# Performance work log

Hardware: AMD Instinct MI355X
Metric: run time of the kernel (lower is better)

The kernel has to match this reference:

```python
import jax, jax.numpy as jnp
import numpy as np


def setup_inputs() -> dict:
    key = jax.random.key(0)
    k1, k2 = jax.random.split(key)
    feat1 = jax.random.normal(k1, (4, 256, 64, 64), dtype=jnp.float32)
    feat2 = jax.random.normal(k2, (4, 256, 64, 64), dtype=jnp.float32)
    return {"feat1": feat1, "feat2": feat2}


def reference(feat1, feat2):
    b, c, h, w = feat1.shape
    hw = h * w
    f1 = feat1.reshape(b, c, hw)  # (b, c, hw)
    f2 = feat2.reshape(b, c, hw)  # (b, c, hw)
    # all-pairs dot-product correlation: corr[b, i, j] = sum_c f1[b,c,i] * f2[b,c,j]
    corr = jnp.einsum('bci,bcj->bij', f1, f2)  # (b, hw, hw)
    # softmax over query-position axis i (torch dim=1)
    out = jax.nn.softmax(corr, axis=1)
    return out.reshape(b, hw, h, w)
```

## Files before the change

kernel.cpp:

```cpp
#include <hip/hip_runtime.h>
#include <math.h>
#include <stdint.h>

#define HW 4096
#define NC 256
#define NB 4
#define NT 32

#define BM 128
#define BN 128
#define BK 32
#define LDP 40

typedef _Float16 f16;
typedef _Float16 half8 __attribute__((ext_vector_type(8)));
typedef float f32x4 __attribute__((ext_vector_type(4)));

#define GLD16(gp, lp) __builtin_amdgcn_global_load_lds( \
    (const __attribute__((address_space(1))) void*)(gp), \
    (__attribute__((address_space(3))) void*)(lp), 16, 0, 0)

__global__ __launch_bounds__(256) void split_tile(const float* __restrict__ src,
                                                  f16* __restrict__ dh,
                                                  f16* __restrict__ dl) {
    const int it = blockIdx.x;
    const int kt = blockIdx.y;
    const int b  = blockIdx.z;
    const float* S = src + (size_t)b * NC * HW + (size_t)kt * 32 * HW + it * 128;

    __shared__ float st[32][133];
    const int t = threadIdx.x;

    {
        const int i4 = (t & 31) * 4;
        const int c0 = t >> 5;
#pragma unroll
        for (int p = 0; p < 4; ++p) {
            const int c = c0 + p * 8;
            const float4 v = *(const float4*)&S[(size_t)c * HW + i4];
            st[c][i4] = v.x; st[c][i4 + 1] = v.y;
            st[c][i4 + 2] = v.z; st[c][i4 + 3] = v.w;
        }
    }
    __syncthreads();

    const size_t tile_base = ((size_t)b * 256 + (size_t)it * 8 + kt) * (128 * 32);
#pragma unroll
    for (int p = 0; p < 2; ++p) {
        const int cid = t + p * 256;
        const int r = cid >> 2, ch = cid & 3;
        f16 h8[8], l8[8];
#pragma unroll
        for (int q = 0; q < 8; ++q) {
            const float x = st[ch * 8 + q][r];
            h8[q] = (f16)x;
            l8[q] = (f16)(x - (float)h8[q]);
        }
        const int off = r * 32 + ((ch ^ ((r >> 1) & 3)) << 3);
        *(half8*)&dh[tile_base + off] = *(half8*)&h8[0];
        *(half8*)&dl[tile_base + off] = *(half8*)&l8[0];
    }
}

__global__ __launch_bounds__(256) void gemm_corr_mfma_t(const f16* __restrict__ Ah,
                                                        const f16* __restrict__ Al,
                                                        const f16* __restrict__ Bh,
                                                        const f16* __restrict__ Bl,
                                                        float* __restrict__ corr,
                                                        f16* __restrict__ p16,
                                                        const int use16,
                                                        float* __restrict__ pm,
                                                        float* __restrict__ ps) {
    const int flat = blockIdx.y * 32 + blockIdx.x;
    const int swz  = (flat & 7) * 128 + (flat >> 3);
    const int it = swz & 31;
    const int jt = swz >> 5;
    const int b  = blockIdx.z;
    const int i0 = it * BM;
    const int j0 = jt * BN;
    float* Cp  = corr + (size_t)b * HW * HW;
    f16*   Pp  = p16  + (size_t)b * HW * HW;

    __shared__ __align__(16) f16 sAh[2 * 4096];
    __shared__ __align__(16) f16 sAl[2 * 4096];
    __shared__ __align__(16) f16 sBh[2 * 4096];
    __shared__ __align__(16) f16 sBl[2 * 4096];

    const int t    = threadIdx.x;
    const int lane = t & 63;
    const int wave = t >> 6;
    const int wr   = (wave >> 1) * 64;
    const int wc   = (wave & 1) * 64;
    const int fm   = lane & 15;
    const int ca   = lane >> 4;

    const size_t abase = ((size_t)b * 256 + (size_t)it * 8) * 4096;
    const size_t bbase = ((size_t)b * 256 + (size_t)jt * 8) * 4096;

    const int swzk = (fm >> 1) & 3;
    const int cswz = ((ca ^ swzk) << 3);
    int aoff[4], boff[4];
#pragma unroll
    for (int u = 0; u < 4; ++u) aoff[u] = (wr + u * 16 + fm) * 32 + cswz;
#pragma unroll
    for (int v = 0; v < 4; ++v) boff[v] = (wc + v * 16 + fm) * 32 + cswz;

    f32x4 acc[4][4];
#pragma unroll
    for (int u = 0; u < 4; ++u)
#pragma unroll
        for (int v = 0; v < 4; ++v) acc[u][v] = (f32x4)(0.f);

    const int stg = wave * 1024 + lane * 8;

#define STAGE(buf, kt_) do {                                             \
        const size_t koff_ = (size_t)(kt_) * 4096;                       \
        _Pragma("unroll")                                                \
        for (int p_ = 0; p_ < 2; ++p_) {                                 \
            const int h_  = stg + p_ * 512;                              \
            const int lb_ = (buf) * 4096 + (wave * 2 + p_) * 512;        \
            GLD16(Ah + abase + koff_ + h_, &sAh[lb_]);                   \
            GLD16(Al + abase + koff_ + h_, &sAl[lb_]);                   \
            GLD16(Bh + bbase + koff_ + h_, &sBh[lb_]);                   \
            GLD16(Bl + bbase + koff_ + h_, &sBl[lb_]);                   \
        }                                                                \
    } while (0)

    STAGE(0, 0);
    __syncthreads();

#pragma unroll
    for (int kt = 0; kt < NC / BK; ++kt) {
        const int cur = kt & 1;
        if (kt < NC / BK - 1) STAGE(cur ^ 1, kt + 1);

        const int cb = cur * 4096;
        half8 fah[4], fal[4], fbh[4], fbl[4];
#pragma unroll
        for (int u = 0; u < 4; ++u) {
            fah[u] = *(const half8*)&sAh[cb + aoff[u]];
            fal[u] = *(const half8*)&sAl[cb + aoff[u]];
        }
#pragma unroll
        for (int v = 0; v < 4; ++v) {
            fbh[v] = *(const half8*)&sBh[cb + boff[v]];
            fbl[v] = *(const half8*)&sBl[cb + boff[v]];
        }
#pragma unroll
        for (int u = 0; u < 4; ++u)
#pragma unroll
            for (int v = 0; v < 4; ++v) {
                acc[u][v] = __builtin_amdgcn_mfma_f32_16x16x32_f16(fah[u], fbh[v], acc[u][v], 0, 0, 0);
                acc[u][v] = __builtin_amdgcn_mfma_f32_16x16x32_f16(fah[u], fbl[v], acc[u][v], 0, 0, 0);
                acc[u][v] = __builtin_amdgcn_mfma_f32_16x16x32_f16(fal[u], fbh[v], acc[u][v], 0, 0, 0);
            }
        __syncthreads();
    }
#undef STAGE

    __syncthreads();
    float* wred = (float*)sAh;

    float mcolv[4];
#pragma unroll
    for (int v = 0; v < 4; ++v) {
        float m16 = -INFINITY;
#pragma unroll
        for (int u = 0; u < 4; ++u)
#pragma unroll
            for (int r = 0; r < 4; ++r) m16 = fmaxf(m16, acc[u][v][r]);
        m16 = fmaxf(m16, __shfl_xor(m16, 16));
        m16 = fmaxf(m16, __shfl_xor(m16, 32));
        if ((lane >> 4) == 0) wred[wave * 64 + v * 16 + fm] = m16;
    }
    __syncthreads();

    const int widx = t >> 6;
    float stat_m = 0.f;
    if (t < BN) stat_m = fmaxf(wred[widx * 64 + (t & 63)],
                               wred[(widx + 2) * 64 + (t & 63)]);
#pragma unroll
    for (int v = 0; v < 4; ++v)
        mcolv[v] = fmaxf(wred[(wave & 1) * 64 + v * 16 + fm],
                         wred[((wave & 1) + 2) * 64 + v * 16 + fm]);
    __syncthreads();

    const int q4 = (lane >> 4) * 4;
#pragma unroll
    for (int v = 0; v < 4; ++v) {
        const int jj = j0 + wc + v * 16 + fm;
        float s16 = 0.f;
        if (use16) {
#pragma unroll
            for (int u = 0; u < 4; ++u)
#pragma unroll
                for (int r = 0; r < 4; ++r) {
                    const int ii = i0 + wr + u * 16 + q4 + r;
                    const f16 ph = (f16)__expf(acc[u][v][r] - mcolv[v]);
                    Pp[(size_t)ii * HW + jj] = ph;
                    s16 += (float)ph;
                }
        } else {
#pragma unroll
            for (int u = 0; u < 4; ++u)
#pragma unroll
                for (int r = 0; r < 4; ++r) {
                    const int ii = i0 + wr + u * 16 + q4 + r;
                    const float pv = __expf(acc[u][v][r] - mcolv[v]);
                    Cp[(size_t)ii * HW + jj] = pv;
                    s16 += pv;
                }
        }
        s16 += __shfl_xor(s16, 16);
        s16 += __shfl_xor(s16, 32);
        if ((lane >> 4) == 0) wred[wave * 64 + v * 16 + fm] = s16;
    }
    __syncthreads();

    if (t < BN) {
        const float s = wred[widx * 64 + (t & 63)] + wred[(widx + 2) * 64 + (t & 63)];
        const int sidx = it * (NB * HW) + b * HW + j0 + t;
        pm[sidx] = stat_m;
        ps[sidx] = s;
    }
}

__global__ __launch_bounds__(256) void gemm_corr_mfma_fb(const float* __restrict__ f1,
                                                         const float* __restrict__ f2,
                                                         float* __restrict__ corr,
                                                         float* __restrict__ pm,
                                                         float* __restrict__ ps) {
    const int i0 = blockIdx.x * BM;
    const int j0 = blockIdx.y * BN;
    const int b  = blockIdx.z;
    const float* Ap = f1 + (size_t)b * NC * HW;
    const float* Bp = f2 + (size_t)b * NC * HW;
    float* Cp = corr + (size_t)b * HW * HW;

    __shared__ __align__(16) f16 Ash[BM * LDP];
    __shared__ __align__(16) f16 Asl[BM * LDP];
    __shared__ __align__(16) f16 Bsh[BN * LDP];
    __shared__ __align__(16) f16 Bsl[BN * LDP];

    const int t    = threadIdx.x;
    const int lane = t & 63;
    const int wave = t >> 6;
    const int wr   = (wave >> 1) * 64;
    const int wc   = (wave & 1) * 64;
    const int si  = t & 127;
    const int sc0 = (t >> 7) * 16;
    const int fm = lane & 15;
    const int fq = (lane >> 4) * 8;

    f32x4 acc[4][4];
#pragma unroll
    for (int u = 0; u < 4; ++u)
#pragma unroll
        for (int v = 0; v < 4; ++v) acc[u][v] = (f32x4)(0.f);

    for (int k0 = 0; k0 < NC; k0 += BK) {
        float av[16], bv[16];
#pragma unroll
        for (int q = 0; q < 16; ++q) {
            const size_t roff = (size_t)(k0 + sc0 + q) * HW;
            av[q] = Ap[roff + i0 + si];
            bv[q] = Bp[roff + j0 + si];
        }
        f16 ah[16], al[16], bh[16], bl[16];
#pragma unroll
        for (int q = 0; q < 16; ++q) {
            ah[q] = (f16)av[q];  al[q] = (f16)(av[q] - (float)ah[q]);
            bh[q] = (f16)bv[q];  bl[q] = (f16)(bv[q] - (float)bh[q]);
        }
        __syncthreads();
        const int wbase = si * LDP + sc0;
        *(half8*)&Ash[wbase]     = *(half8*)&ah[0];
        *(half8*)&Ash[wbase + 8] = *(half8*)&ah[8];
        *(half8*)&Asl[wbase]     = *(half8*)&al[0];
        *(half8*)&Asl[wbase + 8] = *(half8*)&al[8];
        *(half8*)&Bsh[wbase]     = *(half8*)&bh[0];
        *(half8*)&Bsh[wbase + 8] = *(half8*)&bh[8];
        *(half8*)&Bsl[wbase]     = *(half8*)&bl[0];
        *(half8*)&Bsl[wbase + 8] = *(half8*)&bl[8];
        __syncthreads();

        half8 fah[4], fal[4], fbh[4], fbl[4];
#pragma unroll
        for (int u = 0; u < 4; ++u) {
            const int ar = (wr + u * 16 + fm) * LDP + fq;
            fah[u] = *(const half8*)&Ash[ar];
            fal[u] = *(const half8*)&Asl[ar];
        }
#pragma unroll
        for (int v = 0; v < 4; ++v) {
            const int br = (wc + v * 16 + fm) * LDP + fq;
            fbh[v] = *(const half8*)&Bsh[br];
            fbl[v] = *(const half8*)&Bsl[br];
        }
#pragma unroll
        for (int u = 0; u < 4; ++u)
#pragma unroll
            for (int v = 0; v < 4; ++v) {
                acc[u][v] = __builtin_amdgcn_mfma_f32_16x16x32_f16(fah[u], fbh[v], acc[u][v], 0, 0, 0);
                acc[u][v] = __builtin_amdgcn_mfma_f32_16x16x32_f16(fah[u], fbl[v], acc[u][v], 0, 0, 0);
                acc[u][v] = __builtin_amdgcn_mfma_f32_16x16x32_f16(fal[u], fbh[v], acc[u][v], 0, 0, 0);
            }
    }

    __syncthreads();
    float* wred = (float*)Ash;

    float mcolv[4];
#pragma unroll
    for (int v = 0; v < 4; ++v) {
        float m16 = -INFINITY;
#pragma unroll
        for (int u = 0; u < 4; ++u)
#pragma unroll
            for (int r = 0; r < 4; ++r) m16 = fmaxf(m16, acc[u][v][r]);
        m16 = fmaxf(m16, __shfl_xor(m16, 16));
        m16 = fmaxf(m16, __shfl_xor(m16, 32));
        if ((lane >> 4) == 0) wred[wave * 64 + v * 16 + fm] = m16;
    }
    __syncthreads();

    const int widx = t >> 6;
    float stat_m = 0.f;
    if (t < BN) stat_m = fmaxf(wred[widx * 64 + (t & 63)],
                               wred[(widx + 2) * 64 + (t & 63)]);
    float mcv[4];
#pragma unroll
    for (int v = 0; v < 4; ++v)
        mcv[v] = fmaxf(wred[(wave & 1) * 64 + v * 16 + fm],
                       wred[((wave & 1) + 2) * 64 + v * 16 + fm]);
    __syncthreads();

    const int q4 = (lane >> 4) * 4;
#pragma unroll
    for (int v = 0; v < 4; ++v) {
        const int jj = j0 + wc + v * 16 + fm;
        float s16 = 0.f;
#pragma unroll
        for (int u = 0; u < 4; ++u) {
#pragma unroll
            for (int r = 0; r < 4; ++r) {
                const int ii = i0 + wr + u * 16 + q4 + r;
                const float p = __expf(acc[u][v][r] - mcv[v]);
                Cp[(size_t)ii * HW + jj] = p;
                s16 += p;
            }
        }
        s16 += __shfl_xor(s16, 16);
        s16 += __shfl_xor(s16, 32);
        if ((lane >> 4) == 0) wred[wave * 64 + v * 16 + fm] = s16;
    }
    __syncthreads();

    if (t < BN) {
        const float s = wred[widx * 64 + (t & 63)] + wred[(widx + 2) * 64 + (t & 63)];
        const int sidx = blockIdx.x * (NB * HW) + b * HW + j0 + t;
        pm[sidx] = stat_m;
        ps[sidx] = s;
    }
}

__global__ __launch_bounds__(256) void softmax_combine(const float* __restrict__ pm,
                                                       const float* __restrict__ ps,
                                                       float* __restrict__ alpha) {
    const int idx = blockIdx.x * 256 + threadIdx.x;
    float pmv[NT], psv[NT], ec[NT];
    float m = -INFINITY;
#pragma unroll
    for (int c = 0; c < NT; ++c) {
        pmv[c] = pm[c * (NB * HW) + idx];
        psv[c] = ps[c * (NB * HW) + idx];
        m = fmaxf(m, pmv[c]);
    }
    float S = 0.f;
#pragma unroll
    for (int c = 0; c < NT; ++c) {
        ec[c] = __expf(pmv[c] - m);
        S += psv[c] * ec[c];
    }
    const float r = 1.0f / S;
#pragma unroll
    for (int c = 0; c < NT; ++c) alpha[c * (NB * HW) + idx] = ec[c] * r;
}

__global__ __launch_bounds__(256) void softmax_scale16(const f16* __restrict__ p16,
                                                       const float* __restrict__ alpha,
                                                       float* __restrict__ out) {
    const size_t e0 = ((size_t)blockIdx.x * 256 + threadIdx.x) * 8;
    const int b = (int)(e0 >> 24);
    const int i = ((int)(e0 >> 12)) & (HW - 1);
    const int j = ((int)e0) & (HW - 1);
    const float* ap = &alpha[(size_t)(i >> 7) * (NB * HW) + b * HW + j];
    const float4 a0 = *(const float4*)ap;
    const float4 a1 = *(const float4*)(ap + 4);
    const half8 pv = *(const half8*)&p16[e0];
    float4 o0, o1;
    o0.x = (float)pv[0] * a0.x;  o0.y = (float)pv[1] * a0.y;
    o0.z = (float)pv[2] * a0.z;  o0.w = (float)pv[3] * a0.w;
    o1.x = (float)pv[4] * a1.x;  o1.y = (float)pv[5] * a1.y;
    o1.z = (float)pv[6] * a1.z;  o1.w = (float)pv[7] * a1.w;
    *(float4*)&out[e0]     = o0;
    *(float4*)&out[e0 + 4] = o1;
}

__global__ __launch_bounds__(256) void softmax_scale(float* __restrict__ corr,
                                                     const float* __restrict__ alpha) {
    const size_t base = ((size_t)blockIdx.x * 256 + threadIdx.x) * 4;
    const int b = (int)(base >> 24);
    const int i = ((int)(base >> 12)) & (HW - 1);
    const int j = ((int)base) & (HW - 1);
    const float4 a = *(const float4*)&alpha[(size_t)(i >> 7) * (NB * HW) + b * HW + j];
    float4 x = *(float4*)&corr[base];
    x.x *= a.x; x.y *= a.y; x.z *= a.z; x.w *= a.w;
    *(float4*)&corr[base] = x;
}

extern "C" void kernel_launch(void* const* d_in, const int* in_sizes, int n_in,
                              void* d_out, int out_size, void* d_ws, size_t ws_size,
                              hipStream_t stream) {
    const float* f1 = (const float*)d_in[0];
    const float* f2 = (const float*)d_in[1];
    float* out = (float*)d_out;

    float* pm = (float*)d_ws;
    float* ps = pm + NT * NB * HW;
    float* alpha = ps + NT * NB * HW;
    f16* tiles = (f16*)(alpha + NT * NB * HW);
    const size_t tile_elems = (size_t)NB * 256 * 4096;
    f16* Ah = tiles;
    f16* Al = Ah + tile_elems;
    f16* Bh = Al + tile_elems;
    f16* Bl = Bh + tile_elems;
    f16* p16 = Bl + tile_elems;

    const size_t stats_b = 3ull * NT * NB * HW * 4;
    const size_t tiles_b = 4ull * tile_elems * 2;
    const size_t p16_b   = (size_t)NB * HW * HW * 2;

    if (ws_size >= stats_b + tiles_b) {
        const int use16 = (ws_size >= stats_b + tiles_b + p16_b) ? 1 : 0;
        split_tile<<<dim3(HW / BM, NC / BK, NB), 256, 0, stream>>>(f1, Ah, Al);
        split_tile<<<dim3(HW / BM, NC / BK, NB), 256, 0, stream>>>(f2, Bh, Bl);
        gemm_corr_mfma_t<<<dim3(HW / BM, HW / BN, NB), 256, 0, stream>>>(
            Ah, Al, Bh, Bl, out, p16, use16, pm, ps);
        softmax_combine<<<NB * HW / 256, 256, 0, stream>>>(pm, ps, alpha);
        if (use16)
            softmax_scale16<<<(NB * (size_t)HW * HW) / (8 * 256), 256, 0, stream>>>(p16, alpha, out);
        else
            softmax_scale<<<(NB * (size_t)HW * HW) / (4 * 256), 256, 0, stream>>>(out, alpha);
    } else {
        gemm_corr_mfma_fb<<<dim3(HW / BM, HW / BN, NB), 256, 0, stream>>>(
            f1, f2, out, pm, ps);
        softmax_combine<<<NB * HW / 256, 256, 0, stream>>>(pm, ps, alpha);
        softmax_scale<<<(NB * (size_t)HW * HW) / (4 * 256), 256, 0, stream>>>(out, alpha);
    }
}
```

Baseline: 469.2 us.

## Load MFMA fragments directly from global memory instead of LDS staging

The GEMM kernel no longer stages the pre-split fp16 hi/lo tiles through double-buffered shared memory with global_load_lds. Each wave now reads its half8 fragments straight from global memory, relying on L1/L2 caches for reuse. This removes the per-k barriers and frees 64 KB of LDS so that launch_bounds can request 3 blocks per CU. The cost is redundant global or cache traffic, since waves sharing rows re-fetch the same data, and memory latency is no longer hidden by explicit prefetch.

```diff
diff --git a/kernel.cpp b/kernel.cpp
--- a/kernel.cpp
+++ b/kernel.cpp
@@ -15,10 +15,6 @@
 typedef _Float16 f16;
 typedef _Float16 half8 __attribute__((ext_vector_type(8)));
 typedef float f32x4 __attribute__((ext_vector_type(4)));
-
-#define GLD16(gp, lp) __builtin_amdgcn_global_load_lds( \
-    (const __attribute__((address_space(1))) void*)(gp), \
-    (__attribute__((address_space(3))) void*)(lp), 16, 0, 0)
 
 __global__ __launch_bounds__(256) void split_tile(const float* __restrict__ src,
                                                   f16* __restrict__ dh,
@@ -62,15 +58,15 @@
     }
 }
 
-__global__ __launch_bounds__(256) void gemm_corr_mfma_t(const f16* __restrict__ Ah,
-                                                        const f16* __restrict__ Al,
-                                                        const f16* __restrict__ Bh,
-                                                        const f16* __restrict__ Bl,
-                                                        float* __restrict__ corr,
-                                                        f16* __restrict__ p16,
-                                                        const int use16,
-                                                        float* __restrict__ pm,
-                                                        float* __restrict__ ps) {
+__global__ __launch_bounds__(256, 3) void gemm_corr_direct(const f16* __restrict__ Ah,
+                                                           const f16* __restrict__ Al,
+                                                           const f16* __restrict__ Bh,
+                                                           const f16* __restrict__ Bl,
+                                                           float* __restrict__ corr,
+                                                           f16* __restrict__ p16,
+                                                           const int use16,
+                                                           float* __restrict__ pm,
+                                                           float* __restrict__ ps) {
     const int flat = blockIdx.y * 32 + blockIdx.x;
     const int swz  = (flat & 7) * 128 + (flat >> 3);
     const int it = swz & 31;
@@ -81,11 +77,6 @@
     float* Cp  = corr + (size_t)b * HW * HW;
     f16*   Pp  = p16  + (size_t)b * HW * HW;
 
-    __shared__ __align__(16) f16 sAh[2 * 4096];
-    __shared__ __align__(16) f16 sAl[2 * 4096];
-    __shared__ __align__(16) f16 sBh[2 * 4096];
-    __shared__ __align__(16) f16 sBl[2 * 4096];
-
     const int t    = threadIdx.x;
     const int lane = t & 63;
     const int wave = t >> 6;
@@ -94,8 +85,10 @@
     const int fm   = lane & 15;
     const int ca   = lane >> 4;
 
-    const size_t abase = ((size_t)b * 256 + (size_t)it * 8) * 4096;
-    const size_t bbase = ((size_t)b * 256 + (size_t)jt * 8) * 4096;
+    const f16* pAh = Ah + ((size_t)b * 256 + (size_t)it * 8) * 4096;
+    const f16* pAl = Al + ((size_t)b * 256 + (size_t)it * 8) * 4096;
+    const f16* pBh = Bh + ((size_t)b * 256 + (size_t)jt * 8) * 4096;
+    const f16* pBl = Bl + ((size_t)b * 256 + (size_t)jt * 8) * 4096;
 
     const int swzk = (fm >> 1) & 3;
     const int cswz = ((ca ^ swzk) << 3);
@@ -111,40 +104,18 @@
 #pragma unroll
         for (int v = 0; v < 4; ++v) acc[u][v] = (f32x4)(0.f);
 
-    const int stg = wave * 1024 + lane * 8;
-
-#define STAGE(buf, kt_) do {                                             \
-        const size_t koff_ = (size_t)(kt_) * 4096;                       \
-        _Pragma("unroll")                                                \
-        for (int p_ = 0; p_ < 2; ++p_) {                                 \
-            const int h_  = stg + p_ * 512;                              \
-            const int lb_ = (buf) * 4096 + (wave * 2 + p_) * 512;        \
-            GLD16(Ah + abase + koff_ + h_, &sAh[lb_]);                   \
-            GLD16(Al + abase + koff_ + h_, &sAl[lb_]);                   \
-            GLD16(Bh + bbase + koff_ + h_, &sBh[lb_]);                   \
-            GLD16(Bl + bbase + koff_ + h_, &sBl[lb_]);                   \
-        }                                                                \
-    } while (0)
-
-    STAGE(0, 0);
-    __syncthreads();
-
-#pragma unroll
     for (int kt = 0; kt < NC / BK; ++kt) {
-        const int cur = kt & 1;
-        if (kt < NC / BK - 1) STAGE(cur ^ 1, kt + 1);
-
-        const int cb = cur * 4096;
+        const size_t ko = (size_t)kt * 4096;
         half8 fah[4], fal[4], fbh[4], fbl[4];
 #pragma unroll
         for (int u = 0; u < 4; ++u) {
-            fah[u] = *(const half8*)&sAh[cb + aoff[u]];
-            fal[u] = *(const half8*)&sAl[cb + aoff[u]];
+            fah[u] = *(const half8*)&pAh[ko + aoff[u]];
+            fal[u] = *(const half8*)&pAl[ko + aoff[u]];
         }
 #pragma unroll
         for (int v = 0; v < 4; ++v) {
-            fbh[v] = *(const half8*)&sBh[cb + boff[v]];
-            fbl[v] = *(const half8*)&sBl[cb + boff[v]];
+            fbh[v] = *(const half8*)&pBh[ko + boff[v]];
+            fbl[v] = *(const half8*)&pBl[ko + boff[v]];
         }
 #pragma unroll
         for (int u = 0; u < 4; ++u)
@@ -154,12 +125,9 @@
                 acc[u][v] = __builtin_amdgcn_mfma_f32_16x16x32_f16(fah[u], fbl[v], acc[u][v], 0, 0, 0);
                 acc[u][v] = __builtin_amdgcn_mfma_f32_16x16x32_f16(fal[u], fbh[v], acc[u][v], 0, 0, 0);
             }
-        __syncthreads();
-    }
-#undef STAGE
-
-    __syncthreads();
-    float* wred = (float*)sAh;
+    }
+
+    __shared__ float wred[256];
 
     float mcolv[4];
 #pragma unroll
@@ -445,7 +413,7 @@
         const int use16 = (ws_size >= stats_b + tiles_b + p16_b) ? 1 : 0;
         split_tile<<<dim3(HW / BM, NC / BK, NB), 256, 0, stream>>>(f1, Ah, Al);
         split_tile<<<dim3(HW / BM, NC / BK, NB), 256, 0, stream>>>(f2, Bh, Bl);
-        gemm_corr_mfma_t<<<dim3(HW / BM, HW / BN, NB), 256, 0, stream>>>(
+        gemm_corr_direct<<<dim3(HW / BM, HW / BN, NB), 256, 0, stream>>>(
             Ah, Al, Bh, Bl, out, p16, use16, pm, ps);
         softmax_combine<<<NB * HW / 256, 256, 0, stream>>>(pm, ps, alpha);
         if (use16)
```

Result: slower. 522.2 us (+11.3%).
